# Performance work log

Measured on AMD Instinct MI355X. Metric: run time of the kernel, lower is better.

## Reference

```python
import jax, jax.numpy as jnp
import numpy as np

N, E, H_IN, HEADS, C = 50000, 800000, 64, 4, 16


def setup_inputs() -> dict:
    key = jax.random.key(0)
    ks = jax.random.split(key, 9)
    s = 1.0 / np.sqrt(H_IN)
    return {
        "x": jax.random.normal(ks[0], (N, H_IN), jnp.float32),
        "edge_index": jax.random.randint(ks[1], (2, E), 0, N, jnp.int64),
        "W": jax.random.normal(ks[2], (H_IN, HEADS * C), jnp.float32) * s,
        "att_src": jax.random.normal(ks[3], (HEADS, C), jnp.float32) * s,
        "att_dst": jax.random.normal(ks[4], (HEADS, C), jnp.float32) * s,
        "conv_bias": jax.random.normal(ks[5], (HEADS * C,), jnp.float32) * 0.01,
        "skip_W": jax.random.normal(ks[6], (H_IN, HEADS * C), jnp.float32) * s,
        "skip_b": jax.random.normal(ks[7], (HEADS * C,), jnp.float32) * 0.01,
    }


def reference(x, edge_index, W, att_src, att_dst, conv_bias, skip_W, skip_b):
    n = x.shape[0]
    heads, c = att_src.shape
    h = (x @ W).reshape(n, heads, c)                     # [N,H,C]
    a_src = jnp.einsum('nhc,hc->nh', h, att_src)          # [N,H]
    a_dst = jnp.einsum('nhc,hc->nh', h, att_dst)          # [N,H]
    loops = jnp.arange(n, dtype=edge_index.dtype)         # PyG add_self_loops=True
    src = jnp.concatenate([edge_index[0], loops])
    dst = jnp.concatenate([edge_index[1], loops])
    e = jax.nn.leaky_relu(a_src[src] + a_dst[dst], 0.2)   # [E+N,H]
    e_max = jax.ops.segment_max(e, dst, num_segments=n)   # stable segment softmax
    e_exp = jnp.exp(e - e_max[dst])
    denom = jax.ops.segment_sum(e_exp, dst, num_segments=n)
    alpha = e_exp / denom[dst]                            # [E+N,H]
    msg = h[src] * alpha[..., None]                       # [E+N,H,C]
    agg = jax.ops.segment_sum(msg, dst, num_segments=n)   # [N,H,C]
    out = agg.reshape(n, heads * c) + conv_bias
    out = out + x @ skip_W + skip_b                       # residual skip Linear
    # ELU(alpha=0.1)
    return jnp.where(out > 0, out, 0.1 * jnp.expm1(jnp.minimum(out, 0.0)))
```

## Files before the change

kernel.cpp:

```cpp
#include <hip/hip_runtime.h>
#include <hip/hip_bf16.h>
#include <math.h>


#define BLK 256
#define NPB 512
#define NBUCKET 128
#define EPB 2048

typedef __attribute__((ext_vector_type(8))) short short8;
typedef __attribute__((ext_vector_type(4))) float f32x4;

static __device__ __forceinline__ unsigned short f2bf(float f) {
    union { float f; unsigned u; } v; v.f = f;
    return (unsigned short)((v.u + 0x7FFF + ((v.u >> 16) & 1)) >> 16);
}
static __device__ __forceinline__ unsigned short f2fh(float f) {
    union { _Float16 h; unsigned short u; } v; v.h = (_Float16)f; return v.u;
}
static __device__ __forceinline__ float fh2f(unsigned short u) {
    union { _Float16 h; unsigned short u; } v; v.u = u; return (float)v.h;
}

__global__ void prep_weights(const float* __restrict__ W,
                             const float* __restrict__ skipW,
                             const float* __restrict__ conv_bias,
                             const float* __restrict__ skip_b,
                             const float* __restrict__ att_src,
                             const float* __restrict__ att_dst,
                             unsigned short* __restrict__ wfrag,
                             float* __restrict__ bias64,
                             float* __restrict__ watt_s,
                             float* __restrict__ watt_d) {
    const int t = threadIdx.x;
    for (int idx = t; idx < 8192; idx += BLK) {
        const int j = idx & 7;
        const int lane = (idx >> 3) & 63;
        const int kh = (idx >> 9) & 1;
        const int ct = idx >> 10;
        const int k = kh * 32 + (lane >> 4) * 8 + j;
        const int c = ct * 16 + (lane & 15);
        const float v = (c < 64) ? W[k * 64 + c] : skipW[k * 64 + (c - 64)];
        wfrag[idx] = f2bf(v);
    }
    if (t < 64) bias64[t] = conv_bias[t] + skip_b[t];
    {
        const int hh = t >> 6, k = t & 63;
        float ssum = 0.f, dsum = 0.f;
#pragma unroll
        for (int c = 0; c < 16; ++c) {
            const float wv = W[k * 64 + hh * 16 + c];
            ssum = fmaf(wv, att_src[hh * 16 + c], ssum);
            dsum = fmaf(wv, att_dst[hh * 16 + c], dsum);
        }
        watt_s[hh * 64 + k] = ssum;
        watt_d[hh * 64 + k] = dsum;
    }
}

__global__ __launch_bounds__(BLK) void node_bcount(
    const float* __restrict__ x, const unsigned short* __restrict__ wfrag,
    const float* __restrict__ bias64, const float* __restrict__ watt_s,
    const float* __restrict__ watt_d,
    unsigned short* __restrict__ h16, float* __restrict__ base,
    float* __restrict__ a_src, float* __restrict__ a_dst, int n,
    const int* __restrict__ ei_raw, int* __restrict__ blockcnt,
    int n_edges, int nbNode, int nbB, int nbBucket) {
    __shared__ unsigned short sfrag[4 * 64 * 16];
    __shared__ float swatt[512];
    __shared__ int s_is64;
    __shared__ int bh[NBUCKET];
    const int t = threadIdx.x;

    if (blockIdx.x >= nbNode) {
        if (t == 0) {
            int all0 = 1;
            for (int i = 1; i < 128; i += 2) all0 &= (ei_raw[i] == 0);
            s_is64 = all0;
        }
        if (t < NBUCKET) bh[t] = 0;
        __syncthreads();
        const int blk = blockIdx.x - nbNode;
        const int e0 = blk * EPB;
        const int is64 = s_is64;
        const long long* e64 = (const long long*)ei_raw;
#pragma unroll
        for (int i = 0; i < 8; ++i) {
            const int e = e0 + i * BLK + t;
            if (e < n_edges) {
                const int d = is64 ? (int)e64[n_edges + e] : ei_raw[n_edges + e];
                atomicAdd(&bh[d >> 9], 1);
            }
        }
        __syncthreads();
        for (int b = t; b < nbBucket; b += BLK)
            blockcnt[(size_t)b * nbB + blk] = bh[b];
        return;
    }

    const int rowBase = blockIdx.x * 64;

    swatt[t] = watt_s[t];
    swatt[256 + t] = watt_d[t];

    const int r = t >> 2;
    const int c0 = (t & 3) << 4;
    const int grow = rowBase + r;
    float vals[16];
    if (grow < n) {
        const float4* xp = reinterpret_cast<const float4*>(x + (size_t)grow * 64 + c0);
        float4 a0 = xp[0], a1 = xp[1], a2 = xp[2], a3 = xp[3];
        vals[0]=a0.x; vals[1]=a0.y; vals[2]=a0.z; vals[3]=a0.w;
        vals[4]=a1.x; vals[5]=a1.y; vals[6]=a1.z; vals[7]=a1.w;
        vals[8]=a2.x; vals[9]=a2.y; vals[10]=a2.z; vals[11]=a2.w;
        vals[12]=a3.x; vals[13]=a3.y; vals[14]=a3.z; vals[15]=a3.w;
    } else {
#pragma unroll
        for (int i = 0; i < 16; ++i) vals[i] = 0.f;
    }

    {
        const int r15 = r & 15, wv = r >> 4;
#pragma unroll
        for (int oo = 0; oo < 2; ++oo) {
            const int oct = (t & 3) * 2 + oo;
            const int kh = oct >> 2, rg = oct & 3;
            const int lane = rg * 16 + r15;
            short8 p;
#pragma unroll
            for (int i = 0; i < 8; ++i) p[i] = (short)f2bf(vals[oo * 8 + i]);
            *reinterpret_cast<short8*>(&sfrag[((wv * 64 + lane) * 2 + kh) * 8]) = p;
        }
    }
    __syncthreads();

    {
#pragma unroll
        for (int hh = 0; hh < 4; ++hh) {
            float s = 0.f, dd = 0.f;
#pragma unroll
            for (int i = 0; i < 16; ++i) {
                s  = fmaf(vals[i], swatt[hh * 64 + c0 + i], s);
                dd = fmaf(vals[i], swatt[256 + hh * 64 + c0 + i], dd);
            }
            s  += __shfl_xor(s, 1);  s  += __shfl_xor(s, 2);
            dd += __shfl_xor(dd, 1); dd += __shfl_xor(dd, 2);
            if ((t & 3) == 0 && grow < n) {
                a_src[grow * 4 + hh] = s;
                a_dst[grow * 4 + hh] = dd;
            }
        }
    }

    const int wave = t >> 6, lane = t & 63;
    const int q = lane & 15, rg = lane >> 4;

    short8 bfr[8][2];
#pragma unroll
    for (int ct = 0; ct < 8; ++ct)
#pragma unroll
        for (int kh = 0; kh < 2; ++kh)
            bfr[ct][kh] = *reinterpret_cast<const short8*>(
                wfrag + (size_t)((ct * 2 + kh) * 64 + lane) * 8);

    short8 afr[2];
#pragma unroll
    for (int kh = 0; kh < 2; ++kh)
        afr[kh] = *reinterpret_cast<const short8*>(
            &sfrag[((wave * 64 + lane) * 2 + kh) * 8]);

    f32x4 acc[8];
#pragma unroll
    for (int i = 0; i < 8; ++i) { acc[i][0]=0.f; acc[i][1]=0.f; acc[i][2]=0.f; acc[i][3]=0.f; }
#pragma unroll
    for (int ct = 0; ct < 8; ++ct)
#pragma unroll
        for (int kh = 0; kh < 2; ++kh)
            acc[ct] = __builtin_amdgcn_mfma_f32_16x16x32_bf16(
                afr[kh], bfr[ct][kh], acc[ct], 0, 0, 0);

    float biasv[4];
#pragma unroll
    for (int i = 0; i < 4; ++i) biasv[i] = bias64[i * 16 + q];

#pragma unroll
    for (int ct = 0; ct < 4; ++ct)
#pragma unroll
        for (int j = 0; j < 4; ++j) {
            const int gr = rowBase + wave * 16 + rg * 4 + j;
            if (gr < n) h16[(size_t)gr * 64 + ct * 16 + q] = f2fh(acc[ct][j]);
        }
#pragma unroll
    for (int ct = 4; ct < 8; ++ct)
#pragma unroll
        for (int j = 0; j < 4; ++j) {
            const int gr = rowBase + wave * 16 + rg * 4 + j;
            if (gr < n)
                base[(size_t)gr * 64 + (ct - 4) * 16 + q] = acc[ct][j] + biasv[ct - 4];
        }
}

__global__ __launch_bounds__(BLK) void scan1(
    const int* __restrict__ cnt, int* __restrict__ offs,
    int* __restrict__ bsum, int n) {
    __shared__ int s[BLK];
    const int t = threadIdx.x;
    const int gid = blockIdx.x * BLK + t;
    const int v = (gid < n) ? cnt[gid] : 0;
    s[t] = v;
    __syncthreads();
#pragma unroll
    for (int o = 1; o < BLK; o <<= 1) {
        int u = (t >= o) ? s[t - o] : 0;
        __syncthreads();
        s[t] += u;
        __syncthreads();
    }
    if (gid < n) offs[gid] = s[t] - v;
    if (t == BLK - 1) bsum[blockIdx.x] = s[t];
}

__global__ __launch_bounds__(BLK) void scan23(
    int* __restrict__ offs, const int* __restrict__ bsum,
    int n, int total, int nb) {
    __shared__ int sb[BLK];
    const int t = threadIdx.x;
    const int v = (t < nb) ? bsum[t] : 0;
    sb[t] = v;
    __syncthreads();
#pragma unroll
    for (int o = 1; o < BLK; o <<= 1) {
        int u = (t >= o) ? sb[t - o] : 0;
        __syncthreads();
        sb[t] += u;
        __syncthreads();
    }
    sb[t] -= v;
    __syncthreads();
    const int base = sb[blockIdx.x];
    const int gid = blockIdx.x * BLK + t;
    if (gid < n) offs[gid] += base;
    if (gid == 0) offs[n] = total;
}

__global__ __launch_bounds__(BLK) void bucket_write(
    const int* __restrict__ ei_raw, const int* __restrict__ boffs,
    uint2* __restrict__ tmp, int n_edges, int nbB, int nbBucket) {
    __shared__ int s_is64;
    __shared__ int bh[NBUCKET];
    __shared__ int gbase[NBUCKET];
    const int t = threadIdx.x;
    if (t == 0) {
        int all0 = 1;
        for (int i = 1; i < 128; i += 2) all0 &= (ei_raw[i] == 0);
        s_is64 = all0;
    }
    if (t < NBUCKET) bh[t] = 0;
    const int blk = blockIdx.x;
    for (int b = t; b < nbBucket; b += BLK)
        gbase[b] = boffs[(size_t)b * nbB + blk];
    __syncthreads();
    const int e0 = blk * EPB;
    const int is64 = s_is64;
    const long long* e64 = (const long long*)ei_raw;
#pragma unroll
    for (int i = 0; i < 8; ++i) {
        const int e = e0 + i * BLK + t;
        if (e < n_edges) {
            int s, d;
            if (is64) { s = (int)e64[e]; d = (int)e64[n_edges + e]; }
            else      { s = ei_raw[e];   d = ei_raw[n_edges + e]; }
            const int b = d >> 9;
            const int r = atomicAdd(&bh[b], 1);
            tmp[gbase[b] + r] = make_uint2((unsigned)s, (unsigned)d);
        }
    }
}

__global__ __launch_bounds__(BLK) void scatter2(
    const uint2* __restrict__ tmp, const int* __restrict__ boffs,
    int* __restrict__ offs, int* __restrict__ sorted_src,
    int n_nodes, int n_edges, int nbB, int nbBucket) {
    __shared__ int lcnt[NPB];
    __shared__ int lofs[NPB];
    __shared__ int s2[BLK];
    const int b = blockIdx.x;
    const int dbase = b << 9;
    const int ncount = min(NPB, n_nodes - dbase);
    const int t = threadIdx.x;
    const int bucket_base = boffs[(size_t)b * nbB];
    const int next_base = (b + 1 < nbBucket) ? boffs[(size_t)(b + 1) * nbB] : n_edges;
    const int cntb = next_base - bucket_base;

    lcnt[t] = 0; lcnt[t + BLK] = 0;
    __syncthreads();
    const uint2* tb = tmp + bucket_base;
    for (int i = t; i < cntb; i += BLK)
        atomicAdd(&lcnt[(int)tb[i].y - dbase], 1);
    __syncthreads();

    s2[t] = lcnt[2 * t] + lcnt[2 * t + 1];
    __syncthreads();
#pragma unroll
    for (int o = 1; o < BLK; o <<= 1) {
        int u = (t >= o) ? s2[t - o] : 0;
        __syncthreads();
        s2[t] += u;
        __syncthreads();
    }
    const int pbase = (t > 0) ? s2[t - 1] : 0;
    lofs[2 * t] = pbase;
    lofs[2 * t + 1] = pbase + lcnt[2 * t];
    __syncthreads();

    for (int k = t; k < ncount; k += BLK)
        offs[dbase + k] = bucket_base + lofs[k];
    if (b == nbBucket - 1 && t == 0) offs[n_nodes] = n_edges;
    lcnt[t] = 0; lcnt[t + BLK] = 0;
    __syncthreads();

    for (int i = t; i < cntb; i += BLK) {
        const uint2 p = tb[i];
        const int dl = (int)p.y - dbase;
        const int pos = bucket_base + lofs[dl] + atomicAdd(&lcnt[dl], 1);
        sorted_src[pos] = (int)p.x;
    }
}

__global__ __launch_bounds__(BLK) void aggregate_kernel(
    const int* __restrict__ sorted_src, const int* __restrict__ offs,
    const unsigned short* __restrict__ h16,
    const float* __restrict__ a_src, const float* __restrict__ a_dst,
    float* __restrict__ out, int n_nodes) {
    const int g = threadIdx.x >> 4;
    const int q = threadIdx.x & 15;
    const int d = blockIdx.x * 16 + g;
    if (d >= n_nodes) return;
    const int head = q >> 2;
    const float ad = a_dst[d * 4 + head];
    const int beg = offs[d], end = offs[d + 1];

    float e = a_src[d * 4 + head] + ad;
    e = e > 0.f ? e : 0.2f * e;
    const float w = __expf(e);
    float den = w;
    float acc0, acc1, acc2, acc3;
    {
        const ushort4 hp = *reinterpret_cast<const ushort4*>(
            h16 + (size_t)d * 64 + q * 4);
        acc0 = w * fh2f(hp.x); acc1 = w * fh2f(hp.y);
        acc2 = w * fh2f(hp.z); acc3 = w * fh2f(hp.w);
    }

#pragma unroll 4
    for (int j = beg; j < end; ++j) {
        const int s = sorted_src[j];
        float es = a_src[s * 4 + head] + ad;
        es = es > 0.f ? es : 0.2f * es;
        const float ww = __expf(es);
        const ushort4 hp = *reinterpret_cast<const ushort4*>(
            h16 + (size_t)s * 64 + q * 4);
        acc0 = fmaf(ww, fh2f(hp.x), acc0);
        acc1 = fmaf(ww, fh2f(hp.y), acc1);
        acc2 = fmaf(ww, fh2f(hp.z), acc2);
        acc3 = fmaf(ww, fh2f(hp.w), acc3);
        den += ww;
    }

    float* op = out + (size_t)d * 64 + q * 4;
    const float4 b = *reinterpret_cast<const float4*>(op);
    const float inv = 1.f / den;
    float r0 = fmaf(acc0, inv, b.x);
    float r1 = fmaf(acc1, inv, b.y);
    float r2 = fmaf(acc2, inv, b.z);
    float r3 = fmaf(acc3, inv, b.w);
    float4 r;
    r.x = r0 > 0.f ? r0 : 0.1f * expm1f(r0);
    r.y = r1 > 0.f ? r1 : 0.1f * expm1f(r1);
    r.z = r2 > 0.f ? r2 : 0.1f * expm1f(r2);
    r.w = r3 > 0.f ? r3 : 0.1f * expm1f(r3);
    *reinterpret_cast<float4*>(op) = r;
}

extern "C" void kernel_launch(void* const* d_in, const int* in_sizes, int n_in,
                              void* d_out, int out_size, void* d_ws, size_t ws_size,
                              hipStream_t stream) {
    const float* x         = (const float*)d_in[0];
    const int*   ei_raw    = (const int*)d_in[1];
    const float* W         = (const float*)d_in[2];
    const float* att_src   = (const float*)d_in[3];
    const float* att_dst   = (const float*)d_in[4];
    const float* conv_bias = (const float*)d_in[5];
    const float* skip_W    = (const float*)d_in[6];
    const float* skip_b    = (const float*)d_in[7];

    const int n_nodes = in_sizes[0] / 64;
    const int n_edges = in_sizes[1] / 2;

    const int nbNode = (n_nodes + 63) / 64;
    const int nbB = (n_edges + EPB - 1) / EPB;
    const int nbBucket = (n_nodes + NPB - 1) / NPB;
    const int cntN = nbBucket * nbB;
    const int nb_c = (cntN + BLK - 1) / BLK;

    float* ws = (float*)d_ws;
    unsigned short* wfrag = (unsigned short*)ws;
    float* bias64 = ws + 4096;
    float* watt_s = bias64 + 64;
    float* watt_d = watt_s + 256;
    uint2* tmp    = (uint2*)(watt_d + 256);
    unsigned short* h16 = (unsigned short*)(tmp + n_edges);
    float* a_src  = (float*)(h16 + (size_t)n_nodes * 64);
    float* a_dst  = a_src + (size_t)n_nodes * 4;
    int*   blockcnt = (int*)(a_dst + (size_t)n_nodes * 4);
    int*   bsum   = blockcnt + cntN + 1;
    int*   offs   = bsum + 256;
    int*   sorted_src = offs + n_nodes + 1;
    float* base   = (float*)d_out;

    prep_weights<<<1, BLK, 0, stream>>>(W, skip_W, conv_bias, skip_b,
                                        att_src, att_dst, wfrag, bias64,
                                        watt_s, watt_d);

    node_bcount<<<nbNode + nbB, BLK, 0, stream>>>(
        x, wfrag, bias64, watt_s, watt_d, h16, base, a_src, a_dst, n_nodes,
        ei_raw, blockcnt, n_edges, nbNode, nbB, nbBucket);

    scan1<<<nb_c, BLK, 0, stream>>>(blockcnt, blockcnt, bsum, cntN);
    scan23<<<nb_c, BLK, 0, stream>>>(blockcnt, bsum, cntN, n_edges, nb_c);

    bucket_write<<<nbB, BLK, 0, stream>>>(ei_raw, blockcnt, tmp,
                                          n_edges, nbB, nbBucket);
    scatter2<<<nbBucket, BLK, 0, stream>>>(tmp, blockcnt, offs, sorted_src,
                                           n_nodes, n_edges, nbB, nbBucket);

    aggregate_kernel<<<(n_nodes + 15) / 16, BLK, 0, stream>>>(
        sorted_src, offs, h16, a_src, a_dst, (float*)d_out, n_nodes);
}
```

Baseline: 80.46 us.

## Precompute per-edge attention weights in scatter and store them alongside source index

The per-edge leaky-relu and exp of the attention logits moves into the scatter pass. There it is computed once per edge for all four heads and packed as fp16 next to the source index in a 16-byte payload. The aggregate kernel then reads the payload instead of gathering a_src per head per lane and running exp, which removes redundant random gathers and transcendental work. The cost is a 4x larger sorted edge array (16 B vs 4 B per edge) plus extra reads. Rounding the weights to fp16 also loses precision. scatter2 runs only one block per 512-node bucket (98 blocks), so the added per-edge work may serialize there.

```diff
diff --git a/kernel.cpp b/kernel.cpp
--- a/kernel.cpp
+++ b/kernel.cpp
@@ -279,11 +279,13 @@
 
 __global__ __launch_bounds__(BLK) void scatter2(
     const uint2* __restrict__ tmp, const int* __restrict__ boffs,
-    int* __restrict__ offs, int* __restrict__ sorted_src,
+    const float* __restrict__ a_src, const float* __restrict__ a_dst,
+    int* __restrict__ offs, uint4* __restrict__ pay,
     int n_nodes, int n_edges, int nbB, int nbBucket) {
     __shared__ int lcnt[NPB];
     __shared__ int lofs[NPB];
     __shared__ int s2[BLK];
+    __shared__ float sad[NPB * 4];
     const int b = blockIdx.x;
     const int dbase = b << 9;
     const int ncount = min(NPB, n_nodes - dbase);
@@ -293,6 +295,8 @@
     const int cntb = next_base - bucket_base;
 
     lcnt[t] = 0; lcnt[t + BLK] = 0;
+    for (int idx = t; idx < ncount * 4; idx += BLK)
+        sad[idx] = a_dst[dbase * 4 + idx];
     __syncthreads();
     const uint2* tb = tmp + bucket_base;
     for (int i = t; i < cntb; i += BLK)
@@ -321,14 +325,29 @@
 
     for (int i = t; i < cntb; i += BLK) {
         const uint2 p = tb[i];
+        const int s = (int)p.x;
         const int dl = (int)p.y - dbase;
+        const float4 as = *reinterpret_cast<const float4*>(a_src + (size_t)s * 4);
+        float e0 = as.x + sad[dl * 4 + 0];
+        float e1 = as.y + sad[dl * 4 + 1];
+        float e2 = as.z + sad[dl * 4 + 2];
+        float e3 = as.w + sad[dl * 4 + 3];
+        e0 = e0 > 0.f ? e0 : 0.2f * e0;
+        e1 = e1 > 0.f ? e1 : 0.2f * e1;
+        e2 = e2 > 0.f ? e2 : 0.2f * e2;
+        e3 = e3 > 0.f ? e3 : 0.2f * e3;
+        uint4 o;
+        o.x = (unsigned)s;
+        o.y = (unsigned)f2fh(__expf(e0)) | ((unsigned)f2fh(__expf(e1)) << 16);
+        o.z = (unsigned)f2fh(__expf(e2)) | ((unsigned)f2fh(__expf(e3)) << 16);
+        o.w = 0;
         const int pos = bucket_base + lofs[dl] + atomicAdd(&lcnt[dl], 1);
-        sorted_src[pos] = (int)p.x;
+        pay[pos] = o;
     }
 }
 
 __global__ __launch_bounds__(BLK) void aggregate_kernel(
-    const int* __restrict__ sorted_src, const int* __restrict__ offs,
+    const uint4* __restrict__ pay, const int* __restrict__ offs,
     const unsigned short* __restrict__ h16,
     const float* __restrict__ a_src, const float* __restrict__ a_dst,
     float* __restrict__ out, int n_nodes) {
@@ -337,10 +356,9 @@
     const int d = blockIdx.x * 16 + g;
     if (d >= n_nodes) return;
     const int head = q >> 2;
-    const float ad = a_dst[d * 4 + head];
     const int beg = offs[d], end = offs[d + 1];
 
-    float e = a_src[d * 4 + head] + ad;
+    float e = a_src[d * 4 + head] + a_dst[d * 4 + head];
     e = e > 0.f ? e : 0.2f * e;
     const float w = __expf(e);
     float den = w;
@@ -354,12 +372,13 @@
 
 #pragma unroll 4
     for (int j = beg; j < end; ++j) {
-        const int s = sorted_src[j];
-        float es = a_src[s * 4 + head] + ad;
-        es = es > 0.f ? es : 0.2f * es;
-        const float ww = __expf(es);
+        const uint4 p = pay[j];
+        const unsigned pair = (head & 2) ? p.z : p.y;
+        const unsigned short wu =
+            (head & 1) ? (unsigned short)(pair >> 16) : (unsigned short)(pair & 0xffffu);
+        const float ww = fh2f(wu);
         const ushort4 hp = *reinterpret_cast<const ushort4*>(
-            h16 + (size_t)s * 64 + q * 4);
+            h16 + (size_t)(int)p.x * 64 + q * 4);
         acc0 = fmaf(ww, fh2f(hp.x), acc0);
         acc1 = fmaf(ww, fh2f(hp.y), acc1);
         acc2 = fmaf(ww, fh2f(hp.z), acc2);
@@ -408,14 +427,14 @@
     float* bias64 = ws + 4096;
     float* watt_s = bias64 + 64;
     float* watt_d = watt_s + 256;
-    uint2* tmp    = (uint2*)(watt_d + 256);
+    uint4* pay    = (uint4*)(watt_d + 256);
+    uint2* tmp    = (uint2*)(pay + n_edges);
     unsigned short* h16 = (unsigned short*)(tmp + n_edges);
     float* a_src  = (float*)(h16 + (size_t)n_nodes * 64);
     float* a_dst  = a_src + (size_t)n_nodes * 4;
     int*   blockcnt = (int*)(a_dst + (size_t)n_nodes * 4);
     int*   bsum   = blockcnt + cntN + 1;
     int*   offs   = bsum + 256;
-    int*   sorted_src = offs + n_nodes + 1;
     float* base   = (float*)d_out;
 
     prep_weights<<<1, BLK, 0, stream>>>(W, skip_W, conv_bias, skip_b,
@@ -431,9 +450,10 @@
 
     bucket_write<<<nbB, BLK, 0, stream>>>(ei_raw, blockcnt, tmp,
                                           n_edges, nbB, nbBucket);
-    scatter2<<<nbBucket, BLK, 0, stream>>>(tmp, blockcnt, offs, sorted_src,
-                                           n_nodes, n_edges, nbB, nbBucket);
+    scatter2<<<nbBucket, BLK, 0, stream>>>(tmp, blockcnt, a_src, a_dst,
+                                           offs, pay, n_nodes, n_edges,
+                                           nbB, nbBucket);
 
     aggregate_kernel<<<(n_nodes + 15) / 16, BLK, 0, stream>>>(
-        sorted_src, offs, h16, a_src, a_dst, (float*)d_out, n_nodes);
-}
+        pay, offs, h16, a_src, a_dst, (float*)d_out, n_nodes);
+}
```

Measured after the change: 93.04 us. 15.6% more time.
